# Optimization experiments

Measured on AMD Instinct MI355X. Metric: run time of the kernel, lower is better.

Reference implementation:

```python
import jax, jax.numpy as jnp
import numpy as np

D_MODEL = 1024
N_HEADS = 16
D_K = D_MODEL // N_HEADS
MAX_REL = 128
SCALE = float(np.sqrt(D_K))


def setup_inputs() -> dict:
    key = jax.random.key(0)
    ks = jax.random.split(key, 10)
    B, S = 8, 1024
    return {
        "query": jax.random.normal(ks[0], (B, S, D_MODEL), jnp.float32),
        "key": jax.random.normal(ks[1], (B, S, D_MODEL), jnp.float32),
        "value": jax.random.normal(ks[2], (B, S, D_MODEL), jnp.float32),
        "w_q": jax.random.normal(ks[3], (D_MODEL, D_MODEL), jnp.float32) * (1.0 / np.sqrt(D_MODEL)),
        "w_k": jax.random.normal(ks[4], (D_MODEL, D_MODEL), jnp.float32) * (1.0 / np.sqrt(D_MODEL)),
        "w_v": jax.random.normal(ks[5], (D_MODEL, D_MODEL), jnp.float32) * (1.0 / np.sqrt(D_MODEL)),
        "w_o": jax.random.normal(ks[6], (D_MODEL, D_MODEL), jnp.float32) * (1.0 / np.sqrt(D_MODEL)),
        "b_o": jnp.zeros((D_MODEL,), jnp.float32),
        "rel_k": jax.random.normal(ks[7], (2 * MAX_REL + 1, D_K), jnp.float32),
        "rel_v": jax.random.normal(ks[8], (2 * MAX_REL + 1, D_K), jnp.float32),
        "temporal_decay": jnp.ones((N_HEADS,), jnp.float32),
    }


def reference(query, key, value, w_q, w_k, w_v, w_o, b_o, rel_k, rel_v, temporal_decay):
    B, S, D = query.shape
    H, dk = N_HEADS, D_K
    # projections (torch Linear: x @ W.T), reshape to [B,H,S,dk]
    def proj(x, W):
        return (x @ W.T).reshape(B, S, H, dk).transpose(0, 2, 1, 3)
    Q = proj(query, w_q)
    K = proj(key, w_k)
    V = proj(value, w_v)
    scores = jnp.einsum('bhld,bhrd->bhlr', Q, K) / SCALE
    # relative position indices [S,S] in [0, 2*MAX_REL]
    pos = jnp.arange(S)
    rel_idx = jnp.clip(pos[None, :] - pos[:, None], -MAX_REL, MAX_REL) + MAX_REL
    rp_k = rel_k[rel_idx]  # [S,S,dk]
    scores = scores + jnp.einsum('bhld,lrd->bhlr', Q, rp_k)
    # temporal decay bias
    time_dist = jnp.abs(pos[None, :] - pos[:, None]).astype(scores.dtype)  # [S,S]
    scores = scores - temporal_decay[None, :, None, None] * time_dist[None, None]
    attn = jax.nn.softmax(scores, axis=-1)
    context = jnp.einsum('bhlr,bhrd->bhld', attn, V)
    rp_v = rel_v[rel_idx]  # [S,S,dk]
    context = context + jnp.einsum('bhlr,lrd->bhld', attn, rp_v)
    context = context.transpose(0, 2, 1, 3).reshape(B, S, D)
    output = context @ w_o.T + b_o
    return output, attn
```

## Files before the change

kernel.cpp:

```cpp
#include <hip/hip_runtime.h>
#include <cstdint>
#include <cstddef>

#define S_LEN 1024
#define DMODEL 1024
#define NHEADS 16
#define DK 64
#define BATCH 8
#define PUS 296
#define PBS 272
#define RELS 257

using half8_t  = __attribute__((ext_vector_type(8))) _Float16;
using half4_t  = __attribute__((ext_vector_type(4))) _Float16;
using float4_t = __attribute__((ext_vector_type(4))) float;

__device__ __forceinline__ void async16(const void* g, void* l) {
  __builtin_amdgcn_global_load_lds(
      (const __attribute__((address_space(1))) unsigned int*)g,
      (__attribute__((address_space(3))) unsigned int*)l, 16, 0, 0);
}

struct CvtRegion { const float* src; _Float16* dst; int n4; float scale; };
struct CvtArgs { CvtRegion r[8]; };

__global__ __launch_bounds__(256) void cvt_all_kernel(CvtArgs a) {
  CvtRegion reg = a.r[blockIdx.y];
  const int stride = gridDim.x * 256;
  for (int i = blockIdx.x * 256 + threadIdx.x; i < reg.n4; i += stride) {
    float4_t f = ((const float4_t*)reg.src)[i];
    half4_t h;
    h[0] = (_Float16)(f[0] * reg.scale); h[1] = (_Float16)(f[1] * reg.scale);
    h[2] = (_Float16)(f[2] * reg.scale); h[3] = (_Float16)(f[3] * reg.scale);
    ((half4_t*)reg.dst)[i] = h;
  }
}

__global__ void build_rvT_kernel(const float* __restrict__ relv, _Float16* __restrict__ rvT) {
  int d = blockIdx.x;
  int j = threadIdx.x;
  rvT[d * 256 + j] = (j < 255) ? (_Float16)relv[(size_t)(j + 1) * DK + d] : (_Float16)0.f;
}

__device__ __forceinline__ void gemm_core(
    const _Float16* __restrict__ A, const _Float16* __restrict__ B,
    _Float16* smem, float4_t acc[4][4], int m0, int n0,
    int wave, int lane, int quad, int ln, int wm, int wn)
{
  _Float16* As = smem;
  _Float16* Bs = smem + 8192;
#pragma unroll
  for (int i = 0; i < 4; i++)
#pragma unroll
    for (int j = 0; j < 4; j++) { acc[i][j][0]=0.f; acc[i][j][1]=0.f; acc[i][j][2]=0.f; acc[i][j][3]=0.f; }

  for (int k0 = 0; k0 < 1024; k0 += 64) {
#pragma unroll
    for (int q = 0; q < 4; q++) {
      int slot = q * 256 + wave * 64 + lane;
      int m = slot >> 3, g = slot & 7;
      int gg = g ^ (m & 7);
      async16(A + (size_t)(m0 + m) * 1024 + k0 + gg * 8,
              As + (size_t)(q * 256 + wave * 64) * 8);
      async16(B + (size_t)(n0 + m) * 1024 + k0 + gg * 8,
              Bs + (size_t)(q * 256 + wave * 64) * 8);
    }
    __syncthreads();
    half8_t af[4][2], bf[4][2];
#pragma unroll
    for (int t = 0; t < 4; t++) {
      int mm = wm + t * 16 + ln;
      int nn = wn + t * 16 + ln;
#pragma unroll
      for (int kk = 0; kk < 2; kk++) {
        af[t][kk] = *(const half8_t*)(As + mm * 64 + (((kk * 4 + quad) ^ (mm & 7)) * 8));
        bf[t][kk] = *(const half8_t*)(Bs + nn * 64 + (((kk * 4 + quad) ^ (nn & 7)) * 8));
      }
    }
#pragma unroll
    for (int i = 0; i < 4; i++)
#pragma unroll
      for (int j = 0; j < 4; j++) {
        acc[i][j] = __builtin_amdgcn_mfma_f32_16x16x32_f16(af[i][0], bf[j][0], acc[i][j], 0, 0, 0);
        acc[i][j] = __builtin_amdgcn_mfma_f32_16x16x32_f16(af[i][1], bf[j][1], acc[i][j], 0, 0, 0);
      }
    __syncthreads();
  }
}

struct QkvArgs {
  const _Float16* A[3];
  const _Float16* B[3];
  _Float16* dst[3];
};

__global__ __launch_bounds__(256) void gemm_qkv(QkvArgs qa) {
  __shared__ _Float16 smem[16384];
  const int tid = threadIdx.x;
  const int wave = tid >> 6, lane = tid & 63;
  const int quad = lane >> 4, ln = lane & 15;
  const int m0 = blockIdx.x * 128, n0 = blockIdx.y * 128;
  const int wm = (wave >> 1) * 64, wn = (wave & 1) * 64;
  const int z = blockIdx.z;

  float4_t acc[4][4];
  gemm_core(qa.A[z], qa.B[z], smem, acc, m0, n0, wave, lane, quad, ln, wm, wn);

  _Float16* o = qa.dst[z];
  if (z < 2) {
    _Float16* T = smem + wave * 1152;
    size_t headoff = ((size_t)((n0 + wn) >> 6)) << 16;
#pragma unroll
    for (int i = 0; i < 4; i++) {
#pragma unroll
      for (int j = 0; j < 4; j++)
#pragma unroll
        for (int r = 0; r < 4; r++)
          T[(quad * 4 + r) * 72 + j * 16 + ln] = (_Float16)acc[i][j][r];
      int mbase = m0 + wm + i * 16;
#pragma unroll
      for (int p = 0; p < 2; p++) {
        int row = p * 8 + (lane >> 3);
        int cc = (lane & 7) * 8;
        half8_t hv = *(const half8_t*)(T + row * 72 + cc);
        int token = mbase + row;
        size_t idx = ((size_t)(token >> 10) << 20) | headoff
                   | ((size_t)(token & 1023) << 6) | (size_t)cc;
        *(half8_t*)(o + idx) = hv;
      }
    }
  } else {
    _Float16* T = smem + wave * 1160;
    const int tok0 = m0 + wm;
    const size_t base = ((size_t)(tok0 >> 10) << 20)
                      | (((size_t)((n0 + wn) >> 6)) << 16)
                      | (size_t)(tok0 & 1023);
#pragma unroll
    for (int j = 0; j < 4; j++) {
#pragma unroll
      for (int i = 0; i < 4; i++)
#pragma unroll
        for (int r = 0; r < 4; r++)
          T[ln * 72 + i * 16 + quad * 4 + r] = (_Float16)acc[i][j][r];
#pragma unroll
      for (int p = 0; p < 2; p++) {
        int drow = p * 8 + (lane >> 3);
        int cc = (lane & 7) * 8;
        half8_t hv = *(const half8_t*)(T + drow * 72 + cc);
        size_t idx = base + (((size_t)(j * 16 + drow)) << 10) + (size_t)cc;
        *(half8_t*)(o + idx) = hv;
      }
    }
  }
}

__global__ __launch_bounds__(256) void gemm_out(
    const _Float16* __restrict__ A, const _Float16* __restrict__ B,
    float* __restrict__ o, const float* __restrict__ bias)
{
  __shared__ _Float16 smem[16384];
  const int tid = threadIdx.x;
  const int wave = tid >> 6, lane = tid & 63;
  const int quad = lane >> 4, ln = lane & 15;
  const int m0 = blockIdx.x * 128, n0 = blockIdx.y * 128;
  const int wm = (wave >> 1) * 64, wn = (wave & 1) * 64;

  float4_t acc[4][4];
  gemm_core(A, B, smem, acc, m0, n0, wave, lane, quad, ln, wm, wn);

#pragma unroll
  for (int i = 0; i < 4; i++)
#pragma unroll
    for (int j = 0; j < 4; j++) {
      int nn = n0 + wn + j * 16 + ln;
      float bb = bias[nn];
#pragma unroll
      for (int r = 0; r < 4; r++) {
        int mm = m0 + wm + i * 16 + quad * 4 + r;
        o[(size_t)mm * 1024 + nn] = acc[i][j][r] + bb;
      }
    }
}

__global__ __launch_bounds__(256, 4) void attn4_kernel(
    const _Float16* __restrict__ Qh, const _Float16* __restrict__ Kh,
    const _Float16* __restrict__ VtG, const _Float16* __restrict__ relk,
    const _Float16* __restrict__ rvT, const float* __restrict__ decay,
    float* __restrict__ attn_out, _Float16* __restrict__ ctx)
{
  __shared__ float    RelL[16 * RELS];
  __shared__ _Float16 Pu[16 * PUS];
  __shared__ _Float16 Pband[16 * PBS];
  __shared__ float    ctxLds[16 * 64];
  __shared__ float    statsM[4][16];
  __shared__ float    statsZ[4][16];

  const int tid = threadIdx.x;
  const int wave = tid >> 6, lane = tid & 63;
  const int quad = lane >> 4, ln = lane & 15;
  const int bid = blockIdx.x;
  const int b = bid >> 10, h = (bid >> 6) & 15, lt = bid & 63;
  const int l0 = lt * 16;
  const int bh = b * NHEADS + h;
  const _Float16* Qb = Qh + ((size_t)bh << 16);
  const _Float16* Kb = Kh + ((size_t)bh << 16);
  const _Float16* Vb = VtG + ((size_t)bh << 16);
  float* arow = attn_out + ((size_t)bh << 20) + (size_t)l0 * S_LEN;
  const float dec = decay[h];

  const int rlo = (l0 > 127) ? ((l0 - 127) & ~15) : 0;
  int rhi = (l0 + 158) & ~15;
  if (rhi > S_LEN) rhi = S_LEN;
  const int W = rhi - rlo;
  const int nT = W >> 4;
  const int ts = (wave * nT) >> 2;
  const int te = ((wave + 1) * nT) >> 2;

  const float4_t fz = {0.f, 0.f, 0.f, 0.f};
  {
    int w4l = rlo >> 2;
    int w4r = (S_LEN - rhi) >> 2;
#pragma unroll 1
    for (int row = 0; row < 16; row++) {
      float* ar = arow + (size_t)row * S_LEN;
      for (int c4 = tid; c4 < w4l; c4 += 256)
        __builtin_nontemporal_store(fz, (float4_t*)(ar + c4 * 4));
      float* ar2 = ar + rhi;
      for (int c4 = tid; c4 < w4r; c4 += 256)
        __builtin_nontemporal_store(fz, (float4_t*)(ar2 + c4 * 4));
    }
  }
  ((float4_t*)ctxLds)[tid] = fz;
  {
    const half8_t hz = {};
    for (int i = tid; i < 16 * PBS / 8; i += 256) ((half8_t*)Pband)[i] = hz;
    for (int i = tid; i < 16 * PUS / 8; i += 256) ((half8_t*)Pu)[i] = hz;
  }

  half8_t aq[2];
  {
    const _Float16* qp = Qb + (size_t)(l0 + ln) * DK + quad * 8;
    aq[0] = *(const half8_t*)(qp);
    aq[1] = *(const half8_t*)(qp + 32);
  }

#pragma unroll
  for (int s = 0; s < 4; s++) {
    int nt = wave * 4 + s;
    int j = nt * 16 + ln;
    const _Float16* bp = relk + (size_t)(j + 1) * DK + quad * 8;
    half8_t b0 = *(const half8_t*)bp;
    half8_t b1 = *(const half8_t*)(bp + 32);
    float4_t c = {0.f, 0.f, 0.f, 0.f};
    c = __builtin_amdgcn_mfma_f32_16x16x32_f16(aq[0], b0, c, 0, 0, 0);
    c = __builtin_amdgcn_mfma_f32_16x16x32_f16(aq[1], b1, c, 0, 0, 0);
    float db = dec * fabsf((float)(j - 127));
#pragma unroll
    for (int i = 0; i < 4; i++) RelL[(quad * 4 + i) * RELS + j] = c[i] - db;
  }
  __syncthreads();

  float4_t sreg[5];
#pragma unroll
  for (int tt = 0; tt < 5; tt++) { sreg[tt][0]=-1e30f; sreg[tt][1]=-1e30f; sreg[tt][2]=-1e30f; sreg[tt][3]=-1e30f; }

#pragma unroll
  for (int tt = 0; tt < 5; tt++) {
    int t = ts + tt;
    if (t < te) {
      int r0 = rlo + t * 16;
      const _Float16* kp = Kb + (size_t)(r0 + ln) * DK + quad * 8;
      half8_t b0 = *(const half8_t*)(kp);
      half8_t b1 = *(const half8_t*)(kp + 32);
      float4_t c = {0.f, 0.f, 0.f, 0.f};
      c = __builtin_amdgcn_mfma_f32_16x16x32_f16(aq[0], b0, c, 0, 0, 0);
      c = __builtin_amdgcn_mfma_f32_16x16x32_f16(aq[1], b1, c, 0, 0, 0);
      int r = r0 + ln;
#pragma unroll
      for (int i = 0; i < 4; i++) {
        int row = quad * 4 + i;
        int dd = r - (l0 + row);
        bool valid = (dd >= -127) && (dd <= 127);
        sreg[tt][i] = valid ? (c[i] + RelL[row * RELS + (dd + 127)]) : -1e30f;
      }
    }
  }

  float mw[4] = {-1e30f, -1e30f, -1e30f, -1e30f};
#pragma unroll
  for (int tt = 0; tt < 5; tt++)
#pragma unroll
    for (int i = 0; i < 4; i++) mw[i] = fmaxf(mw[i], sreg[tt][i]);
#pragma unroll
  for (int off = 1; off < 16; off <<= 1)
#pragma unroll
    for (int i = 0; i < 4; i++) mw[i] = fmaxf(mw[i], __shfl_xor(mw[i], off, 64));

  float ew[4] = {0.f, 0.f, 0.f, 0.f};
#pragma unroll
  for (int tt = 0; tt < 5; tt++)
#pragma unroll
    for (int i = 0; i < 4; i++) {
      float e = (sreg[tt][i] > -1e29f) ? __expf(sreg[tt][i] - mw[i]) : 0.f;
      sreg[tt][i] = e;
      ew[i] += e;
    }
#pragma unroll
  for (int off = 1; off < 16; off <<= 1)
#pragma unroll
    for (int i = 0; i < 4; i++) ew[i] += __shfl_xor(ew[i], off, 64);

  if (ln == 0) {
#pragma unroll
    for (int i = 0; i < 4; i++) {
      statsM[wave][quad * 4 + i] = mw[i];
      statsZ[wave][quad * 4 + i] = ew[i];
    }
  }
  __syncthreads();

  float scale[4];
#pragma unroll
  for (int i = 0; i < 4; i++) {
    int row = quad * 4 + i;
    float mf = fmaxf(fmaxf(statsM[0][row], statsM[1][row]),
                     fmaxf(statsM[2][row], statsM[3][row]));
    float z = statsZ[0][row] * __expf(statsM[0][row] - mf)
            + statsZ[1][row] * __expf(statsM[1][row] - mf)
            + statsZ[2][row] * __expf(statsM[2][row] - mf)
            + statsZ[3][row] * __expf(statsM[3][row] - mf);
    scale[i] = __expf(mw[i] - mf) / z;
  }

#pragma unroll
  for (int tt = 0; tt < 5; tt++) {
    int t = ts + tt;
    if (t < te) {
      int col = t * 16 + ln;
      int r = rlo + col;
#pragma unroll
      for (int i = 0; i < 4; i++) {
        int row = quad * 4 + i;
        _Float16 ph = (_Float16)(sreg[tt][i] * scale[i]);
        Pu[row * PUS + col] = ph;
        int dd = r - (l0 + row);
        if (dd >= -127 && dd <= 127) Pband[row * PBS + (dd + 127)] = ph;
      }
    }
  }
  __syncthreads();

  {
    int row = tid >> 4;
    int lc = tid & 15;
    float* ar = arow + (size_t)row * S_LEN + rlo;
    const _Float16* pr = Pu + row * PUS;
    int W4 = W >> 2;
    for (int c4 = lc; c4 < W4; c4 += 16) {
      half4_t hp = *(const half4_t*)(pr + c4 * 4);
      float4_t f;
      f[0] = (float)hp[0]; f[1] = (float)hp[1];
      f[2] = (float)hp[2]; f[3] = (float)hp[3];
      __builtin_nontemporal_store(f, (float4_t*)(ar + c4 * 4));
    }
  }

  float4_t ctxa[4];
#pragma unroll
  for (int nt = 0; nt < 4; nt++) { ctxa[nt][0]=0.f; ctxa[nt][1]=0.f; ctxa[nt][2]=0.f; ctxa[nt][3]=0.f; }
  {
    int nC = (W + 31) >> 5;
    int cs = (wave * nC) >> 2, ce = ((wave + 1) * nC) >> 2;
    for (int cc2 = cs; cc2 < ce; cc2++) {
      half8_t a = *(const half8_t*)(Pu + ln * PUS + cc2 * 32 + quad * 8);
      int rb = rlo + cc2 * 32 + quad * 8;
#pragma unroll
      for (int nt = 0; nt < 4; nt++) {
        half8_t bv = *(const half8_t*)(Vb + (size_t)(nt * 16 + ln) * S_LEN + rb);
        ctxa[nt] = __builtin_amdgcn_mfma_f32_16x16x32_f16(a, bv, ctxa[nt], 0, 0, 0);
      }
    }
  }
#pragma unroll
  for (int nt = 0; nt < 4; nt++)
#pragma unroll
    for (int i = 0; i < 4; i++)
      atomicAdd(&ctxLds[(quad * 4 + i) * 64 + nt * 16 + ln], ctxa[nt][i]);
  __syncthreads();

  {
    float4_t rc = {0.f, 0.f, 0.f, 0.f};
#pragma unroll
    for (int cch = 0; cch < 8; cch++) {
      half8_t apb = *(const half8_t*)(Pband + ln * PBS + cch * 32 + quad * 8);
      half8_t bb  = *(const half8_t*)(rvT + (size_t)(wave * 16 + ln) * 256 + cch * 32 + quad * 8);
      rc = __builtin_amdgcn_mfma_f32_16x16x32_f16(apb, bb, rc, 0, 0, 0);
    }
#pragma unroll
    for (int i = 0; i < 4; i++)
      ctxLds[(quad * 4 + i) * 64 + wave * 16 + ln] += rc[i];
  }
  __syncthreads();

  {
    int l = tid >> 4, d4 = (tid & 15) * 4;
    const float* cs = ctxLds + l * 64 + d4;
    half4_t hv;
    hv[0] = (_Float16)cs[0]; hv[1] = (_Float16)cs[1];
    hv[2] = (_Float16)cs[2]; hv[3] = (_Float16)cs[3];
    *(half4_t*)(ctx + ((size_t)(b * S_LEN + l0 + l)) * DMODEL + h * DK + d4) = hv;
  }
}

extern "C" void kernel_launch(void* const* d_in, const int* in_sizes, int n_in,
                              void* d_out, int out_size, void* d_ws, size_t ws_size,
                              hipStream_t stream) {
  const float* q   = (const float*)d_in[0];
  const float* k   = (const float*)d_in[1];
  const float* v   = (const float*)d_in[2];
  const float* wq  = (const float*)d_in[3];
  const float* wk  = (const float*)d_in[4];
  const float* wv  = (const float*)d_in[5];
  const float* wo  = (const float*)d_in[6];
  const float* bo  = (const float*)d_in[7];
  const float* rk  = (const float*)d_in[8];
  const float* rv  = (const float*)d_in[9];
  const float* td  = (const float*)d_in[10];

  char* ws = (char*)d_ws;
  size_t off = 0;
  auto alloc = [&](size_t bytes) -> void* {
    void* p = ws + off;
    off += (bytes + 255) & ~(size_t)255;
    return p;
  };
  const size_t NTOK = (size_t)BATCH * S_LEN;
  _Float16* Xq  = (_Float16*)alloc(NTOK * DMODEL * 2);
  _Float16* Xk  = (_Float16*)alloc(NTOK * DMODEL * 2);
  _Float16* Xv  = (_Float16*)alloc(NTOK * DMODEL * 2);
  _Float16* Wqh = (_Float16*)alloc((size_t)DMODEL * DMODEL * 2);
  _Float16* Wkh = (_Float16*)alloc((size_t)DMODEL * DMODEL * 2);
  _Float16* Wvh = (_Float16*)alloc((size_t)DMODEL * DMODEL * 2);
  _Float16* Woh = (_Float16*)alloc((size_t)DMODEL * DMODEL * 2);
  _Float16* Qh  = (_Float16*)alloc(NTOK * DMODEL * 2);
  _Float16* Kh  = (_Float16*)alloc(NTOK * DMODEL * 2);
  _Float16* VtG = (_Float16*)alloc(NTOK * DMODEL * 2 + 256);
  _Float16* Ctx = (_Float16*)alloc(NTOK * DMODEL * 2);
  _Float16* Rkh = (_Float16*)alloc((size_t)257 * 64 * 2);
  _Float16* RvT = (_Float16*)alloc((size_t)64 * 256 * 2);

  CvtArgs ca;
  ca.r[0] = {q,  Xq,  (int)(NTOK * DMODEL / 4), 1.f};
  ca.r[1] = {k,  Xk,  (int)(NTOK * DMODEL / 4), 1.f};
  ca.r[2] = {v,  Xv,  (int)(NTOK * DMODEL / 4), 1.f};
  ca.r[3] = {wq, Wqh, DMODEL * DMODEL / 4, 0.125f};
  ca.r[4] = {wk, Wkh, DMODEL * DMODEL / 4, 1.f};
  ca.r[5] = {wv, Wvh, DMODEL * DMODEL / 4, 1.f};
  ca.r[6] = {wo, Woh, DMODEL * DMODEL / 4, 1.f};
  ca.r[7] = {rk, Rkh, 257 * 64 / 4, 8.f};
  cvt_all_kernel<<<dim3(512, 8), dim3(256), 0, stream>>>(ca);
  build_rvT_kernel<<<dim3(64), dim3(256), 0, stream>>>(rv, RvT);

  QkvArgs qa;
  qa.A[0] = Xq; qa.A[1] = Xk; qa.A[2] = Xv;
  qa.B[0] = Wqh; qa.B[1] = Wkh; qa.B[2] = Wvh;
  qa.dst[0] = Qh; qa.dst[1] = Kh; qa.dst[2] = VtG;
  gemm_qkv<<<dim3(64, 8, 3), dim3(256), 0, stream>>>(qa);

  float* attn_out = (float*)d_out + NTOK * DMODEL;
  attn4_kernel<<<dim3(BATCH * NHEADS * (S_LEN / 16)), dim3(256), 0, stream>>>(
      Qh, Kh, VtG, Rkh, RvT, td, attn_out, Ctx);

  gemm_out<<<dim3(64, 8), dim3(256), 0, stream>>>(Ctx, Woh, (float*)d_out, bo);
}
```

Baseline: 932.5 us.

## Replace LDS atomic context reduction with per-wave slabs and remap blocks to XCDs

The attention kernel no longer reduces the context accumulators with LDS atomicAdd into a shared buffer followed by an extra barrier. Each wave instead writes its partial context tile into its own LDS slab, and the slabs are summed at the final fp16 store. The relative-position band contribution is folded into the registers before that store. The slab buffer reuses the RelL storage, which removes the separate ctxLds array. Blocks are also remapped so each group of eight consecutive block IDs covers different batches. The aim is for each XCD to keep one batch's K/V resident in its L2. The cost is one more slab read per output element and a dependence on the earlier barriers before the RelL space is reused.

```diff
diff --git a/kernel.cpp b/kernel.cpp
--- a/kernel.cpp
+++ b/kernel.cpp
@@ -10,6 +10,7 @@
 #define PUS 296
 #define PBS 272
 #define RELS 257
+#define SLABS 68
 
 using half8_t  = __attribute__((ext_vector_type(8))) _Float16;
 using half4_t  = __attribute__((ext_vector_type(4))) _Float16;
@@ -188,17 +189,17 @@
     const _Float16* __restrict__ rvT, const float* __restrict__ decay,
     float* __restrict__ attn_out, _Float16* __restrict__ ctx)
 {
-  __shared__ float    RelL[16 * RELS];
+  __shared__ float    scratch[4 * 16 * SLABS];
   __shared__ _Float16 Pu[16 * PUS];
   __shared__ _Float16 Pband[16 * PBS];
-  __shared__ float    ctxLds[16 * 64];
   __shared__ float    statsM[4][16];
   __shared__ float    statsZ[4][16];
 
   const int tid = threadIdx.x;
   const int wave = tid >> 6, lane = tid & 63;
   const int quad = lane >> 4, ln = lane & 15;
-  const int bid = blockIdx.x;
+  const int hw = blockIdx.x;
+  const int bid = ((hw & 7) << 10) | (hw >> 3);
   const int b = bid >> 10, h = (bid >> 6) & 15, lt = bid & 63;
   const int l0 = lt * 16;
   const int bh = b * NHEADS + h;
@@ -230,7 +231,6 @@
         __builtin_nontemporal_store(fz, (float4_t*)(ar2 + c4 * 4));
     }
   }
-  ((float4_t*)ctxLds)[tid] = fz;
   {
     const half8_t hz = {};
     for (int i = tid; i < 16 * PBS / 8; i += 256) ((half8_t*)Pband)[i] = hz;
@@ -256,7 +256,7 @@
     c = __builtin_amdgcn_mfma_f32_16x16x32_f16(aq[1], b1, c, 0, 0, 0);
     float db = dec * fabsf((float)(j - 127));
 #pragma unroll
-    for (int i = 0; i < 4; i++) RelL[(quad * 4 + i) * RELS + j] = c[i] - db;
+    for (int i = 0; i < 4; i++) scratch[(quad * 4 + i) * RELS + j] = c[i] - db;
   }
   __syncthreads();
 
@@ -281,7 +281,7 @@
         int row = quad * 4 + i;
         int dd = r - (l0 + row);
         bool valid = (dd >= -127) && (dd <= 127);
-        sreg[tt][i] = valid ? (c[i] + RelL[row * RELS + (dd + 127)]) : -1e30f;
+        sreg[tt][i] = valid ? (c[i] + scratch[row * RELS + (dd + 127)]) : -1e30f;
       }
     }
   }
@@ -381,12 +381,6 @@
       }
     }
   }
-#pragma unroll
-  for (int nt = 0; nt < 4; nt++)
-#pragma unroll
-    for (int i = 0; i < 4; i++)
-      atomicAdd(&ctxLds[(quad * 4 + i) * 64 + nt * 16 + ln], ctxa[nt][i]);
-  __syncthreads();
 
   {
     float4_t rc = {0.f, 0.f, 0.f, 0.f};
@@ -396,18 +390,34 @@
       half8_t bb  = *(const half8_t*)(rvT + (size_t)(wave * 16 + ln) * 256 + cch * 32 + quad * 8);
       rc = __builtin_amdgcn_mfma_f32_16x16x32_f16(apb, bb, rc, 0, 0, 0);
     }
-#pragma unroll
-    for (int i = 0; i < 4; i++)
-      ctxLds[(quad * 4 + i) * 64 + wave * 16 + ln] += rc[i];
+    if (wave == 0)      { ctxa[0][0]+=rc[0]; ctxa[0][1]+=rc[1]; ctxa[0][2]+=rc[2]; ctxa[0][3]+=rc[3]; }
+    else if (wave == 1) { ctxa[1][0]+=rc[0]; ctxa[1][1]+=rc[1]; ctxa[1][2]+=rc[2]; ctxa[1][3]+=rc[3]; }
+    else if (wave == 2) { ctxa[2][0]+=rc[0]; ctxa[2][1]+=rc[1]; ctxa[2][2]+=rc[2]; ctxa[2][3]+=rc[3]; }
+    else                { ctxa[3][0]+=rc[0]; ctxa[3][1]+=rc[1]; ctxa[3][2]+=rc[2]; ctxa[3][3]+=rc[3]; }
+  }
+
+  {
+    float* slab = scratch + wave * (16 * SLABS);
+#pragma unroll
+    for (int nt = 0; nt < 4; nt++)
+#pragma unroll
+      for (int i = 0; i < 4; i++)
+        slab[(quad * 4 + i) * SLABS + nt * 16 + ln] = ctxa[nt][i];
   }
   __syncthreads();
 
   {
     int l = tid >> 4, d4 = (tid & 15) * 4;
-    const float* cs = ctxLds + l * 64 + d4;
+    const float* s0 = scratch + l * SLABS + d4;
+    float4_t v0 = *(const float4_t*)(s0);
+    float4_t v1 = *(const float4_t*)(s0 + 16 * SLABS);
+    float4_t v2 = *(const float4_t*)(s0 + 32 * SLABS);
+    float4_t v3 = *(const float4_t*)(s0 + 48 * SLABS);
     half4_t hv;
-    hv[0] = (_Float16)cs[0]; hv[1] = (_Float16)cs[1];
-    hv[2] = (_Float16)cs[2]; hv[3] = (_Float16)cs[3];
+    hv[0] = (_Float16)(v0[0] + v1[0] + v2[0] + v3[0]);
+    hv[1] = (_Float16)(v0[1] + v1[1] + v2[1] + v3[1]);
+    hv[2] = (_Float16)(v0[2] + v1[2] + v2[2] + v3[2]);
+    hv[3] = (_Float16)(v0[3] + v1[3] + v2[3] + v3[3]);
     *(half4_t*)(ctx + ((size_t)(b * S_LEN + l0 + l)) * DMODEL + h * DK + d4) = hv;
   }
 }
```

Result: faster. 793.8 us (-14.9%).
